# Performance work log

Hardware: AMD Instinct MI355X
Metric: run time of the kernel (lower is better)

## Reference

```python
import jax, jax.numpy as jnp
import numpy as np

KNN = 11  # self.knn in VoronoiBaseNN


def setup_inputs() -> dict:
    key = jax.random.key(0)
    k1, k2 = jax.random.split(key)
    points = jax.random.normal(k1, (2, 50000, 3), dtype=jnp.float32)   # GT surface samples
    spoints = jax.random.normal(k2, (2, 4000, 3), dtype=jnp.float32)   # Voronoi generators
    return {"points": points, "spoints": spoints}


def reference(points, spoints):
    # Pairwise squared distances: [B, N, M]
    d2 = ((points[:, :, None, :] - spoints[:, None, :, :]) ** 2).sum(-1)
    # KNN smallest, sorted ascending (torch.topk(largest=False, sorted=True))
    _, idx = jax.lax.top_k(-d2, KNN)            # idx: [B, N, KNN]
    # Gather the KNN generator coordinates: [B, N, KNN, 3]
    gathered = jax.vmap(lambda sp, i: sp[i])(spoints, idx)
    inside = gathered[:, :, 0, :]               # closest cell center [B, N, 3]
    point_to_center = points - inside           # [B, N, 3]
    # Voronoi edge vectors to the other KNN-1 neighbors: [B, N, KNN-1, 3]
    voronoi_edge = gathered[:, :, 1:, :] - inside[:, :, None, :]
    edge_l = jnp.sqrt((voronoi_edge ** 2).sum(-1))                      # [B, N, KNN-1]
    vector_length = (point_to_center[:, :, None, :] * voronoi_edge).sum(-1) / edge_l
    sq_dist = (vector_length - edge_l / 2.0) ** 2
    return sq_dist.min(-1)                      # [B, N]
```

## Files before the change

kernel.cpp:

```cpp
#include <hip/hip_runtime.h>
#include <math.h>

#define NPTS  50000
#define NSP   4000
#define NGRP  1000
#define NW    8
#define QW    (NGRP / NW)
#define KNN   11
#define BIG   3.4e38f
#define SEGCAP 96
#define SEGPAD 8
#define SEGSTR (SEGCAP + SEGPAD)
#define GRIDC 32
#define NKEY  65536
#define NGB   ((NPTS + 63) / 64)

#define MED3(a,b,c) __builtin_amdgcn_fmed3f((a),(b),(c))

__device__ unsigned g_hist[NKEY];
__device__ float4   g_sorted[2 * NPTS];

static __device__ __forceinline__ unsigned spread5(unsigned v) {
    return (v & 1u) | ((v & 2u) << 2) | ((v & 4u) << 4) |
           ((v & 8u) << 6) | ((v & 16u) << 8);
}

static __device__ __forceinline__ unsigned cell_key(int b, float x, float y, float z) {
    int gx = (int)floorf((x + 4.0f) * 4.0f);
    int gy = (int)floorf((y + 4.0f) * 4.0f);
    int gz = (int)floorf((z + 4.0f) * 4.0f);
    gx = min(max(gx, 0), GRIDC - 1);
    gy = min(max(gy, 0), GRIDC - 1);
    gz = min(max(gz, 0), GRIDC - 1);
    unsigned m = spread5((unsigned)gx) | (spread5((unsigned)gy) << 1) |
                 (spread5((unsigned)gz) << 2);
    return ((unsigned)b << 15) | m;
}

__global__ void k_zero() {
    int t = blockIdx.x * 256 + threadIdx.x;
    if (t < NKEY) g_hist[t] = 0u;
}
__global__ void k_hist(const float* __restrict__ pts) {
    int n = blockIdx.x * 256 + threadIdx.x;
    if (n >= 2 * NPTS) return;
    const float* p = pts + (size_t)n * 3;
    int b = (n >= NPTS) ? 1 : 0;
    atomicAdd(&g_hist[cell_key(b, p[0], p[1], p[2])], 1u);
}
__global__ void k_scan() {
    __shared__ unsigned part[1024];
    const int t = threadIdx.x;
    const unsigned base = (unsigned)blockIdx.x * 32768u + (unsigned)t * 32u;
    unsigned s = 0;
#pragma unroll
    for (int j = 0; j < 32; ++j) s += g_hist[base + j];
    part[t] = s;
    __syncthreads();
    for (int off = 1; off < 1024; off <<= 1) {
        unsigned v = (t >= off) ? part[t - off] : 0u;
        __syncthreads();
        part[t] += v;
        __syncthreads();
    }
    unsigned run = (unsigned)blockIdx.x * (unsigned)NPTS + part[t] - s;
#pragma unroll
    for (int j = 0; j < 32; ++j) {
        unsigned h = g_hist[base + j];
        g_hist[base + j] = run;
        run += h;
    }
}
__global__ void k_scatter(const float* __restrict__ pts) {
    int n = blockIdx.x * 256 + threadIdx.x;
    if (n >= 2 * NPTS) return;
    const float* p = pts + (size_t)n * 3;
    int b = (n >= NPTS) ? 1 : 0;
    float x = p[0], y = p[1], z = p[2];
    unsigned dst = atomicAdd(&g_hist[cell_key(b, x, y, z)], 1u);
    if (dst < 2u * NPTS)
        g_sorted[dst] = make_float4(x, y, z, __uint_as_float((unsigned)(n - b * NPTS)));
}

static __device__ __forceinline__ float wred_min(float v) {
#pragma unroll
    for (int off = 32; off > 0; off >>= 1) v = fminf(v, __shfl_xor(v, off, 64));
    return v;
}
static __device__ __forceinline__ float wred_max(float v) {
#pragma unroll
    for (int off = 32; off > 0; off >>= 1) v = fmaxf(v, __shfl_xor(v, off, 64));
    return v;
}

__global__ __launch_bounds__(512, 6) void voronoi_kernel(
    const float* __restrict__ spts,
    float* __restrict__ out)
{
    __shared__ float4 sl[NW * SEGSTR];
    __shared__ float  lds_d[NW][64][11];
    __shared__ int    lds_i[NW][64];
    __shared__ float  lds_b[NW][64];
    __shared__ float  lds_m[NW];

    const int b    = blockIdx.y;
    const int lane = threadIdx.x & 63;
    const int wq   = threadIdx.x >> 6;
    const int grp  = (int)(((unsigned)blockIdx.x * 401u) % (unsigned)NGB);
    int pi = grp * 64 + lane;
    const bool valid = (pi < NPTS);
    if (!valid) pi = NPTS - 1;

    const float4 P = g_sorted[(size_t)b * NPTS + pi];
    const float px = P.x, py = P.y, pz = P.z;
    const unsigned orig = __float_as_uint(P.w);

    const float mnx = wred_min(px), mxx = wred_max(px);
    const float mny = wred_min(py), mxy = wred_max(py);
    const float mnz = wred_min(pz), mxz = wred_max(pz);
    const float ccx = 0.5f * (mnx + mxx);
    const float ccy = 0.5f * (mny + mxy);
    const float ccz = 0.5f * (mnz + mxz);
    const float R = sqrtf(wred_max(
        fmaf(px - ccx, px - ccx, fmaf(py - ccy, py - ccy, (pz - ccz) * (pz - ccz)))));

    const float4* __restrict__ spq = (const float4*)(spts + (size_t)b * NSP * 3);
    const int g0 = wq * QW, g1 = g0 + QW;

    float myMin = BIG;
    for (int k0 = g0; k0 < g1; k0 += 64) {
        const int g  = k0 + lane;
        const int gc = (g < g1) ? g : (g1 - 1);
        const float4 q0 = spq[3 * gc + 0];
        const float4 q1 = spq[3 * gc + 1];
        const float4 q2 = spq[3 * gc + 2];
        float dx = q0.x - ccx, dy = q0.y - ccy, dz = q0.z - ccz;
        float md = fmaf(dx, dx, fmaf(dy, dy, dz * dz));
        dx = q0.w - ccx; dy = q1.x - ccy; dz = q1.y - ccz;
        md = fminf(md, fmaf(dx, dx, fmaf(dy, dy, dz * dz)));
        dx = q1.z - ccx; dy = q1.w - ccy; dz = q2.x - ccz;
        md = fminf(md, fmaf(dx, dx, fmaf(dy, dy, dz * dz)));
        dx = q2.y - ccx; dy = q2.z - ccy; dz = q2.w - ccz;
        md = fminf(md, fmaf(dx, dx, fmaf(dy, dy, dz * dz)));
        if (g < g1) myMin = fminf(myMin, md);
    }
    float vv = myMin, m11 = 0.0f;
#pragma unroll
    for (int t = 0; t < KNN; ++t) {
        m11 = wred_min(vv);
        vv = (vv == m11) ? BIG : vv;
    }
    if (lane == 0) lds_m[wq] = m11;
    __syncthreads();
    float m11g = BIG;
#pragma unroll
    for (int q = 0; q < NW; ++q) m11g = fminf(m11g, lds_m[q]);
    const float Trad = sqrtf(m11g) + R;
    const float T = Trad * Trad * 1.0004f + 1e-12f;

#define ADM(sx, sy, sz) \
    (fmaf(MED3((sx), mnx, mxx) - (sx), MED3((sx), mnx, mxx) - (sx), \
     fmaf(MED3((sy), mny, mxy) - (sy), MED3((sy), mny, mxy) - (sy), \
          (MED3((sz), mnz, mxz) - (sz)) * (MED3((sz), mnz, mxz) - (sz)))) <= T)

    const int segbase = wq * SEGSTR;
    unsigned cnt = 0;

    auto padseg = [&]() {
        if (lane < SEGPAD)
            sl[segbase + (int)cnt + lane] =
                make_float4(1e18f, 1e18f, 1e18f, __uint_as_float(0x7fffffffu));
    };

#define PUSH(sx, sy, sz, ok, idx, CONSUME) { \
        const unsigned long long msk = __ballot(ok); \
        const unsigned np = (unsigned)__popcll(msk); \
        if (cnt + np > (unsigned)SEGCAP) {               \
            padseg(); CONSUME(cnt); cnt = 0; of = true; \
        } \
        if (ok) { \
            const unsigned pos = cnt + \
                __builtin_amdgcn_mbcnt_hi((unsigned)(msk >> 32), \
                    __builtin_amdgcn_mbcnt_lo((unsigned)msk, 0u)); \
            sl[segbase + (int)pos] = \
                make_float4((sx), (sy), (sz), __uint_as_float((unsigned)(idx))); \
        } \
        cnt += np; }

#define RUN_BUILD(CONSUME, ofvar) { \
        ofvar = false; bool& of = ofvar; cnt = 0; \
        for (int k0 = g0; k0 < g1; k0 += 64) { \
            const int g  = k0 + lane; \
            const int gc = (g < g1) ? g : (g1 - 1); \
            const bool in = (g < g1); \
            const float4 q0 = spq[3 * gc + 0]; \
            const float4 q1 = spq[3 * gc + 1]; \
            const float4 q2 = spq[3 * gc + 2]; \
            const bool a0 = in && ADM(q0.x, q0.y, q0.z); \
            const bool a1 = in && ADM(q0.w, q1.x, q1.y); \
            const bool a2 = in && ADM(q1.z, q1.w, q2.x); \
            const bool a3 = in && ADM(q2.y, q2.z, q2.w); \
            PUSH(q0.x, q0.y, q0.z, a0, 4 * gc + 0, CONSUME); \
            PUSH(q0.w, q1.x, q1.y, a1, 4 * gc + 1, CONSUME); \
            PUSH(q1.z, q1.w, q2.x, a2, 4 * gc + 2, CONSUME); \
            PUSH(q2.y, q2.z, q2.w, a3, 4 * gc + 3, CONSUME); \
        } \
        padseg(); CONSUME(cnt); }

    float d0 = BIG, d1 = BIG, d2 = BIG, d3 = BIG, d4 = BIG, d5 = BIG,
          d6 = BIG, d7 = BIG, d8 = BIG, d9 = BIG, d10 = BIG;
    int i0 = 0x7fffffff;

#define CHAIN(nd, jj) { \
        if (__ballot((nd) < d10)) { \
            d10 = MED3(d9, d10, (nd)); \
            d9  = MED3(d8, d9,  (nd)); \
            d8  = MED3(d7, d8,  (nd)); \
            d7  = MED3(d6, d7,  (nd)); \
            d6  = MED3(d5, d6,  (nd)); \
            d5  = MED3(d4, d5,  (nd)); \
            d4  = MED3(d3, d4,  (nd)); \
            d3  = MED3(d2, d3,  (nd)); \
            d2  = MED3(d1, d2,  (nd)); \
            d1  = MED3(d0, d1,  (nd)); \
            i0  = ((nd) < d0) ? (jj) : i0; \
            d0  = fminf(d0, (nd)); \
        } }
#define CANDA(c) { \
        const float dx = px - (c).x, dy = py - (c).y, dz = pz - (c).z; \
        const float nd = fmaf(dx, dx, fmaf(dy, dy, dz * dz)); \
        const int jj = (int)__float_as_uint((c).w); \
        CHAIN(nd, jj); }

    auto chainA = [&](unsigned n) {
        if (n == 0u) return;
        float4 e0 = sl[segbase + 0], e1 = sl[segbase + 1],
               e2 = sl[segbase + 2], e3 = sl[segbase + 3];
        for (unsigned k = 0; k < n; k += 4) {
            const float4 n0 = sl[segbase + (int)k + 4];
            const float4 n1 = sl[segbase + (int)k + 5];
            const float4 n2 = sl[segbase + (int)k + 6];
            const float4 n3 = sl[segbase + (int)k + 7];
            CANDA(e0); CANDA(e1); CANDA(e2); CANDA(e3);
            e0 = n0; e1 = n1; e2 = n2; e3 = n3;
        }
    };

    bool ovfA;
    RUN_BUILD(chainA, ovfA);
    const unsigned cntA = cnt;

    lds_d[wq][lane][0]  = d0;  lds_d[wq][lane][1]  = d1;
    lds_d[wq][lane][2]  = d2;  lds_d[wq][lane][3]  = d3;
    lds_d[wq][lane][4]  = d4;  lds_d[wq][lane][5]  = d5;
    lds_d[wq][lane][6]  = d6;  lds_d[wq][lane][7]  = d7;
    lds_d[wq][lane][8]  = d8;  lds_d[wq][lane][9]  = d9;
    lds_d[wq][lane][10] = d10;
    lds_i[wq][lane] = i0;
    __syncthreads();

    float gb = BIG; int gi = 0x7fffffff;
#pragma unroll
    for (int q = 0; q < NW; ++q) {
        const float dq = lds_d[q][lane][0];
        const int   iq = lds_i[q][lane];
        const bool take = (dq < gb) || (dq == gb && iq < gi);
        gb = take ? dq : gb;
        gi = take ? iq : gi;
    }
#define INS(v) { \
        d10 = MED3(d9, d10, (v)); \
        d9  = MED3(d8, d9,  (v)); \
        d8  = MED3(d7, d8,  (v)); \
        d7  = MED3(d6, d7,  (v)); \
        d6  = MED3(d5, d6,  (v)); \
        d5  = MED3(d4, d5,  (v)); \
        d4  = MED3(d3, d4,  (v)); \
        d3  = MED3(d2, d3,  (v)); \
        d2  = MED3(d1, d2,  (v)); \
        d1  = MED3(d0, d1,  (v)); \
        d0  = fminf(d0, (v)); }
#pragma unroll
    for (int q = 0; q < NW; ++q) {
        if (q == wq) continue;
#pragma unroll
        for (int k = 0; k < 11; ++k) {
            const float v = lds_d[q][lane][k];
            if (!__ballot(v < d10)) break;
            INS(v);
        }
    }
    const float d10g = d10;
    const int   i0g  = gi;

    const float* ip = spts + (size_t)b * NSP * 3 + (size_t)(unsigned)i0g * 3;
    const float ix = ip[0], iy = ip[1], iz = ip[2];
    const float vx = px - ix, vy = py - iy, vz = pz - iz;
    float best = BIG;

#define CANDB(c) { \
        const float dx = px - (c).x, dy = py - (c).y, dz = pz - (c).z; \
        const float nd = fmaf(dx, dx, fmaf(dy, dy, dz * dz)); \
        const int jj = (int)__float_as_uint((c).w); \
        const bool adm = (nd <= d10g) && (jj != i0g); \
        if (__ballot(adm)) { \
            const float ex = (c).x - ix, ey = (c).y - iy, ez = (c).z - iz; \
            const float ee = fmaf(ex, ex, fmaf(ey, ey, ez * ez)); \
            const float dt = fmaf(vx, ex, fmaf(vy, ey, vz * ez)); \
            const float u  = fmaf(-0.5f, ee, dt); \
            const float t2 = u * u * __builtin_amdgcn_rcpf(ee); \
            best = adm ? fminf(best, t2) : best; \
        } }

    auto scanB = [&](unsigned n) {
        if (n == 0u) return;
        float4 e0 = sl[segbase + 0], e1 = sl[segbase + 1],
               e2 = sl[segbase + 2], e3 = sl[segbase + 3];
        for (unsigned k = 0; k < n; k += 4) {
            const float4 n0 = sl[segbase + (int)k + 4];
            const float4 n1 = sl[segbase + (int)k + 5];
            const float4 n2 = sl[segbase + (int)k + 6];
            const float4 n3 = sl[segbase + (int)k + 7];
            CANDB(e0); CANDB(e1); CANDB(e2); CANDB(e3);
            e0 = n0; e1 = n1; e2 = n2; e3 = n3;
        }
    };

    if (!ovfA) {
        scanB(cntA);
    } else {
        bool ovfB;
        RUN_BUILD(scanB, ovfB);
        (void)ovfB;
    }

    lds_b[wq][lane] = best;
    __syncthreads();
    if (wq == 0) {
        float m = lds_b[0][lane];
#pragma unroll
        for (int q = 1; q < NW; ++q) m = fminf(m, lds_b[q][lane]);
        if (valid) out[(size_t)b * NPTS + orig] = m;
    }
}

extern "C" void kernel_launch(void* const* d_in, const int* in_sizes, int n_in,
                              void* d_out, int out_size, void* d_ws, size_t ws_size,
                              hipStream_t stream) {
    (void)in_sizes; (void)n_in; (void)d_ws; (void)ws_size; (void)out_size;
    const float* pts  = (const float*)d_in[0];
    const float* spts = (const float*)d_in[1];
    float* out = (float*)d_out;

    k_zero   <<<dim3(NKEY / 256),            dim3(256),  0, stream>>>();
    k_hist   <<<dim3((2 * NPTS + 255)/256),  dim3(256),  0, stream>>>(pts);
    k_scan   <<<dim3(2),                     dim3(1024), 0, stream>>>();
    k_scatter<<<dim3((2 * NPTS + 255)/256),  dim3(256),  0, stream>>>(pts);
    voronoi_kernel<<<dim3(NGB, 2), dim3(512), 0, stream>>>(spts, out);
}
```

Before: 260.2 us.

## Fuse histogram, scan and scatter into one LDS-resident per-batch sort kernel

Replaces the four-kernel global-memory counting sort (zero, histogram, scan, scatter) with a single kernel that uses one 1024-thread workgroup per batch and keeps a 32768-bin histogram in 128 KB of LDS. This removes three launches and the global atomics, at the cost of running the sort on only two workgroups, so little of the GPU is busy during it. The old path stays as a fallback if the launch fails. Separately, the voronoi kernel reuses the lds_i array for its final reduction buffer to cut shared memory, with an extra barrier added before the reuse.

Result: slower. 285.1 us (+9.6%).

```diff
diff --git a/kernel.cpp b/kernel.cpp
--- a/kernel.cpp
+++ b/kernel.cpp
@@ -24,17 +24,60 @@
     return (v & 1u) | ((v & 2u) << 2) | ((v & 4u) << 4) |
            ((v & 8u) << 6) | ((v & 16u) << 8);
 }
-
-static __device__ __forceinline__ unsigned cell_key(int b, float x, float y, float z) {
+static __device__ __forceinline__ unsigned morton15(float x, float y, float z) {
     int gx = (int)floorf((x + 4.0f) * 4.0f);
     int gy = (int)floorf((y + 4.0f) * 4.0f);
     int gz = (int)floorf((z + 4.0f) * 4.0f);
     gx = min(max(gx, 0), GRIDC - 1);
     gy = min(max(gy, 0), GRIDC - 1);
     gz = min(max(gz, 0), GRIDC - 1);
-    unsigned m = spread5((unsigned)gx) | (spread5((unsigned)gy) << 1) |
-                 (spread5((unsigned)gz) << 2);
-    return ((unsigned)b << 15) | m;
+    return spread5((unsigned)gx) | (spread5((unsigned)gy) << 1) |
+           (spread5((unsigned)gz) << 2);
+}
+
+__global__ __launch_bounds__(1024, 1) void k_sort(const float* __restrict__ pts) {
+    __shared__ unsigned h[32768];
+    __shared__ unsigned ps[1024];
+    const int b = blockIdx.x;
+    const int t = threadIdx.x;
+    const float* __restrict__ pb = pts + (size_t)b * NPTS * 3;
+
+#pragma unroll
+    for (int i = 0; i < 32; ++i) h[t + i * 1024] = 0u;
+    __syncthreads();
+
+    for (int n = t; n < NPTS; n += 1024) {
+        const float x = pb[n * 3], y = pb[n * 3 + 1], z = pb[n * 3 + 2];
+        atomicAdd(&h[morton15(x, y, z)], 1u);
+    }
+    __syncthreads();
+
+    unsigned s = 0;
+#pragma unroll
+    for (int j = 0; j < 32; ++j) s += h[t * 32 + j];
+    ps[t] = s;
+    __syncthreads();
+    for (int off = 1; off < 1024; off <<= 1) {
+        const unsigned v = (t >= off) ? ps[t - off] : 0u;
+        __syncthreads();
+        ps[t] += v;
+        __syncthreads();
+    }
+    unsigned run = ps[t] - s;
+#pragma unroll
+    for (int j = 0; j < 32; ++j) {
+        const unsigned c = h[t * 32 + j];
+        h[t * 32 + j] = run;
+        run += c;
+    }
+    __syncthreads();
+
+    for (int n = t; n < NPTS; n += 1024) {
+        const float x = pb[n * 3], y = pb[n * 3 + 1], z = pb[n * 3 + 2];
+        const unsigned dst = atomicAdd(&h[morton15(x, y, z)], 1u);
+        g_sorted[(size_t)b * NPTS + dst] =
+            make_float4(x, y, z, __uint_as_float((unsigned)n));
+    }
 }
 
 __global__ void k_zero() {
@@ -46,7 +89,7 @@
     if (n >= 2 * NPTS) return;
     const float* p = pts + (size_t)n * 3;
     int b = (n >= NPTS) ? 1 : 0;
-    atomicAdd(&g_hist[cell_key(b, p[0], p[1], p[2])], 1u);
+    atomicAdd(&g_hist[((unsigned)b << 15) | morton15(p[0], p[1], p[2])], 1u);
 }
 __global__ void k_scan() {
     __shared__ unsigned part[1024];
@@ -77,7 +120,7 @@
     const float* p = pts + (size_t)n * 3;
     int b = (n >= NPTS) ? 1 : 0;
     float x = p[0], y = p[1], z = p[2];
-    unsigned dst = atomicAdd(&g_hist[cell_key(b, x, y, z)], 1u);
+    unsigned dst = atomicAdd(&g_hist[((unsigned)b << 15) | morton15(x, y, z)], 1u);
     if (dst < 2u * NPTS)
         g_sorted[dst] = make_float4(x, y, z, __uint_as_float((unsigned)(n - b * NPTS)));
 }
@@ -100,8 +143,9 @@
     __shared__ float4 sl[NW * SEGSTR];
     __shared__ float  lds_d[NW][64][11];
     __shared__ int    lds_i[NW][64];
-    __shared__ float  lds_b[NW][64];
     __shared__ float  lds_m[NW];
+
+    float (*lds_b)[64] = (float (*)[64])lds_i;
 
     const int b    = blockIdx.y;
     const int lane = threadIdx.x & 63;
@@ -334,6 +378,7 @@
         (void)ovfB;
     }
 
+    __syncthreads();
     lds_b[wq][lane] = best;
     __syncthreads();
     if (wq == 0) {
@@ -352,9 +397,13 @@
     const float* spts = (const float*)d_in[1];
     float* out = (float*)d_out;
 
-    k_zero   <<<dim3(NKEY / 256),            dim3(256),  0, stream>>>();
-    k_hist   <<<dim3((2 * NPTS + 255)/256),  dim3(256),  0, stream>>>(pts);
-    k_scan   <<<dim3(2),                     dim3(1024), 0, stream>>>();
-    k_scatter<<<dim3((2 * NPTS + 255)/256),  dim3(256),  0, stream>>>(pts);
+    (void)hipGetLastError();
+    k_sort<<<dim3(2), dim3(1024), 0, stream>>>(pts);
+    if (hipGetLastError() != hipSuccess) {
+        k_zero   <<<dim3(NKEY / 256),            dim3(256),  0, stream>>>();
+        k_hist   <<<dim3((2 * NPTS + 255)/256),  dim3(256),  0, stream>>>(pts);
+        k_scan   <<<dim3(2),                     dim3(1024), 0, stream>>>();
+        k_scatter<<<dim3((2 * NPTS + 255)/256),  dim3(256),  0, stream>>>(pts);
+    }
     voronoi_kernel<<<dim3(NGB, 2), dim3(512), 0, stream>>>(spts, out);
 }
```
